# Kernel tuning notes

Hardware: AMD Instinct MI355X
Metric: run time of the kernel (lower is better)

## Reference

```python
import jax, jax.numpy as jnp
import numpy as np

# ---- static geometry / topology tables (the CUDA kernel's x,y,z,inner tables) ----
W = D = H = 49                     # vertex grid
Wc, Dc, Hc = W - 1, D - 1, H - 1    # cell grid
N_CELLS = Wc * Dc * Hc
T_FULL = 96                         # number of topology classes in `topology`
T_TRI = 48                          # triangle-bearing topologies (topology_to_triangles)
EPS = 1e-8

# 12 cube edges: (corner where edge starts, axis the edge runs along)
EDGE_CORNER = np.array([
    [0,0,0],[0,1,0],[0,0,1],[0,1,1],   # x-edges
    [0,0,0],[1,0,0],[0,0,1],[1,0,1],   # y-edges
    [0,0,0],[1,0,0],[0,1,0],[1,1,0],   # z-edges
], dtype=np.int32)
EDGE_AXIS = np.array([0,0,0,0,1,1,1,1,2,2,2,2], dtype=np.int32)

_rng = np.random.default_rng(0)
# per triangle-topology: the 3 cube edges carrying its triangle vertices
TRI_TABLE = np.stack([_rng.choice(12, size=3, replace=False) for _ in range(T_TRI)]).astype(np.int32)
# columns of `topology` that correspond to triangle topologies
TT_IDX = np.sort(_rng.choice(T_FULL, size=T_TRI, replace=False)).astype(np.int32)


def _triangle_normals(offset):
    """offset: [3, W, D, H] -> unit normals [T_TRI, Wc, Dc, Hc, 3]."""
    verts = []
    for e in range(12):
        cx, cy, cz = EDGE_CORNER[e]
        ax = int(EDGE_AXIS[e])
        # displacement of the MC vertex along its edge, gathered per cell
        disp = offset[ax, cx:cx + Wc, cy:cy + Dc, cz:cz + Hc]   # [Wc,Dc,Hc]
        base = np.array([cx, cy, cz], dtype=np.float32)
        base[ax] += 0.5                                          # edge midpoint
        unit = np.zeros(3, dtype=np.float32); unit[ax] = 1.0
        # cell-local vertex position (cell origin cancels in edge differences)
        verts.append(jnp.asarray(base) + disp[..., None] * jnp.asarray(unit))
    verts = jnp.stack(verts)                                     # [12,Wc,Dc,Hc,3]
    v0 = verts[TRI_TABLE[:, 0]]                                  # [T_TRI,Wc,Dc,Hc,3]
    v1 = verts[TRI_TABLE[:, 1]]
    v2 = verts[TRI_TABLE[:, 2]]
    n = jnp.cross(v1 - v0, v2 - v0)
    n = n / jnp.sqrt(jnp.sum(n * n, axis=-1, keepdims=True) + EPS)
    return n


def _curvature_loss(offset, topology):
    n = _triangle_normals(offset)                                # [T,Wc,Dc,Hc,3]
    p = topology[:, TT_IDX].reshape(Wc, Dc, Hc, T_TRI)           # per-cell topo probs
    s = jnp.sum(p, axis=-1)                                      # [Wc,Dc,Hc]
    m = jnp.einsum('xyzt,txyzc->xyzc', p, n)                     # prob-weighted normal sum

    # sum_{t1,t2} p1 p2 ||n1 - n2||^2 = 2*(s1*s2 - m1.m2) for unit normals
    def pair(sa, ma, sb, mb):
        return jnp.sum(2.0 * (sa * sb - jnp.sum(ma * mb, axis=-1)))

    loss_x = pair(s[:-1], m[:-1], s[1:], m[1:])
    loss_y = pair(s[:, :-1], m[:, :-1], s[:, 1:], m[:, 1:])
    loss_z = pair(s[:, :, :-1], m[:, :, :-1], s[:, :, 1:], m[:, :, 1:])
    loss_inner = pair(s, m, s, m)
    return loss_x + loss_y + loss_z + loss_inner


def setup_inputs() -> dict:
    key = jax.random.key(0)
    k1, k2 = jax.random.split(key)
    offset = 0.1 * jax.random.normal(k1, (3, W, D, H), dtype=jnp.float32)
    topology = jax.random.uniform(k2, (N_CELLS, T_FULL), dtype=jnp.float32)
    return {"offset": offset, "topology": topology}


def reference(offset, topology):
    return _curvature_loss(offset, topology)
```

## Files before the change

### kernel.cpp

```cpp
#include <hip/hip_runtime.h>
#include <cstdint>

#define NCELLS (48*48*48)
#define NT 48
#define CB 64
#define NW 8
#define PITCH 97
#define OFFE 882

namespace nprng {
typedef unsigned __int128 u128;
struct PCG { u128 state; u128 inc; int has32; uint32_t cached; };

constexpr u128 mult128() {
  return (((u128)2549297995355413924ULL) << 64) | (u128)4865540595714422341ULL;
}
constexpr void step(PCG& g) { g.state = g.state * mult128() + g.inc; }
constexpr uint64_t out64(const PCG& g) {
  uint64_t x = (uint64_t)(g.state >> 64) ^ (uint64_t)g.state;
  unsigned rot = (unsigned)(g.state >> 122);
  return (x >> rot) | (x << ((64u - rot) & 63u));
}
constexpr uint64_t next64(PCG& g) { step(g); return out64(g); }
constexpr uint32_t next32(PCG& g) {
  if (g.has32) { g.has32 = 0; return g.cached; }
  uint64_t v = next64(g);
  g.has32 = 1; g.cached = (uint32_t)(v >> 32);
  return (uint32_t)v;
}
constexpr uint32_t lemire32(PCG& g, uint32_t rngmax) {
  const uint32_t rng_excl = rngmax + 1u;
  uint64_t m = (uint64_t)next32(g) * (uint64_t)rng_excl;
  uint32_t leftover = (uint32_t)m;
  if (leftover < rng_excl) {
    const uint32_t threshold = (uint32_t)((0xFFFFFFFFu - rngmax) % rng_excl);
    while (leftover < threshold) {
      m = (uint64_t)next32(g) * (uint64_t)rng_excl;
      leftover = (uint32_t)m;
    }
  }
  return (uint32_t)(m >> 32);
}
constexpr uint64_t rbu(PCG& g, uint64_t rngmax) {
  if (rngmax == 0) return 0;
  return (uint64_t)lemire32(g, (uint32_t)rngmax);
}
constexpr uint32_t hashmix(uint32_t v, uint32_t& hc) {
  v ^= hc; hc *= 0x931e8875u; v *= hc; v ^= v >> 16; return v;
}
constexpr uint32_t mix2(uint32_t x, uint32_t y) {
  uint32_t r = 0xca01f9ddu * x - 0x4973f715u * y; r ^= r >> 16; return r;
}
constexpr PCG seed_pcg0() {
  PCG g{0, 0, 0, 0};
  uint32_t pool[4] = {};
  uint32_t hc = 0x43b0d7e5u;
  for (int i = 0; i < 4; i++) pool[i] = hashmix(0u, hc);
  for (int s = 0; s < 4; s++)
    for (int d = 0; d < 4; d++)
      if (s != d) pool[d] = mix2(pool[d], hashmix(pool[s], hc));
  uint32_t st[8] = {};
  uint32_t hb = 0x8b51f9ddu;
  for (int i = 0; i < 8; i++) {
    uint32_t v = pool[i & 3];
    v ^= hb; hb *= 0x58f38dedu; v *= hb; v ^= v >> 16;
    st[i] = v;
  }
  uint64_t w[4] = {};
  for (int i = 0; i < 4; i++) w[i] = (uint64_t)st[2 * i] | ((uint64_t)st[2 * i + 1] << 32);
  u128 initstate = (((u128)w[0]) << 64) | (u128)w[1];
  u128 initseq   = (((u128)w[2]) << 64) | (u128)w[3];
  g.state = 0; g.inc = (initseq << 1) | (u128)1;
  step(g); g.state += initstate; step(g);
  g.has32 = 0; g.cached = 0;
  return g;
}
constexpr void choice_nr(PCG& g, int pop, int n, int* outv, bool shuf) {
  uint64_t hs[64] = {};
  uint64_t set_size = (uint64_t)(1.2 * (double)n);
  uint64_t mask = set_size;
  mask |= mask >> 1; mask |= mask >> 2; mask |= mask >> 4;
  mask |= mask >> 8; mask |= mask >> 16; mask |= mask >> 32;
  for (int i = 0; i < 64; i++) hs[i] = ~0ULL;
  for (int j = pop - n; j < pop; j++) {
    uint64_t val = rbu(g, (uint64_t)j);
    uint64_t loc = val & mask;
    while (hs[loc] != ~0ULL && hs[loc] != val) loc = (loc + 1) & mask;
    if (hs[loc] == ~0ULL) { hs[loc] = val; outv[j - (pop - n)] = (int)val; }
    else {
      loc = (uint64_t)j & mask;
      while (hs[loc] != ~0ULL) loc = (loc + 1) & mask;
      hs[loc] = (uint64_t)j;
      outv[j - (pop - n)] = j;
    }
  }
  if (shuf) {
    for (int i = n - 1; i >= 1; i--) {
      uint64_t j = rbu(g, (uint64_t)i);
      int t = outv[i]; outv[i] = outv[(int)j]; outv[(int)j] = t;
    }
  }
}
}

struct TriTab3 {
  float ub[NT][3];
  float wb[NT][3];
  int   a0[NT], a1[NT], a2[NT];
  int   lofc[NT][3];
  int   tto[NT];
};

constexpr TriTab3 make_tab() {
  TriTab3 T{};
  nprng::PCG g = nprng::seed_pcg0();
  int tri[NT][3] = {};
  for (int t = 0; t < NT; t++) nprng::choice_nr(g, 12, 3, tri[t], true);
  int tt[NT] = {};
  nprng::choice_nr(g, 96, NT, tt, true);
  for (int i = 1; i < NT; i++) {
    int v = tt[i], j = i - 1;
    while (j >= 0 && tt[j] > v) { tt[j + 1] = tt[j]; j--; }
    tt[j + 1] = v;
  }
  constexpr int EC[12][3] = {{0,0,0},{0,1,0},{0,0,1},{0,1,1},
                             {0,0,0},{1,0,0},{0,0,1},{1,0,1},
                             {0,0,0},{1,0,0},{0,1,0},{1,1,0}};
  constexpr int EA[12] = {0,0,0,0,1,1,1,1,2,2,2,2};
  for (int t = 0; t < NT; t++) {
    float B[3][3] = {};
    int ax[3] = {};
    for (int k = 0; k < 3; k++) {
      int e = tri[t][k];
      int a = EA[e];
      ax[k] = a;
      T.lofc[t][k] = ((a * 2 + EC[e][0]) * 3 + EC[e][1]) * 49 + EC[e][2];
      B[k][0] = (float)EC[e][0]; B[k][1] = (float)EC[e][1]; B[k][2] = (float)EC[e][2];
      B[k][a] += 0.5f;
    }
    for (int c = 0; c < 3; c++) {
      T.ub[t][c] = B[1][c] - B[0][c];
      T.wb[t][c] = B[2][c] - B[0][c];
    }
    T.a0[t] = ax[0]; T.a1[t] = ax[1]; T.a2[t] = ax[2];
    T.tto[t] = tt[t];
  }
  return T;
}

static constexpr TriTab3 TAB = make_tab();

template <int t>
__device__ __forceinline__ void do1(const float* __restrict__ loff, int lanebase,
                                    const float* __restrict__ myrow,
                                    float& s, float& mx, float& my, float& mz) {
  constexpr int L0 = TAB.lofc[t][0], L1 = TAB.lofc[t][1], L2 = TAB.lofc[t][2];
  constexpr int A0 = TAB.a0[t], A1 = TAB.a1[t], A2 = TAB.a2[t];
  float p  = myrow[TAB.tto[t]];
  float d0 = loff[lanebase + L0];
  float d1 = loff[lanebase + L1];
  float d2 = loff[lanebase + L2];
  float ux = TAB.ub[t][0] + (A1 == 0 ? d1 : 0.0f) - (A0 == 0 ? d0 : 0.0f);
  float uy = TAB.ub[t][1] + (A1 == 1 ? d1 : 0.0f) - (A0 == 1 ? d0 : 0.0f);
  float uz = TAB.ub[t][2] + (A1 == 2 ? d1 : 0.0f) - (A0 == 2 ? d0 : 0.0f);
  float wx = TAB.wb[t][0] + (A2 == 0 ? d2 : 0.0f) - (A0 == 0 ? d0 : 0.0f);
  float wy = TAB.wb[t][1] + (A2 == 1 ? d2 : 0.0f) - (A0 == 1 ? d0 : 0.0f);
  float wz = TAB.wb[t][2] + (A2 == 2 ? d2 : 0.0f) - (A0 == 2 ? d0 : 0.0f);
  float cxv = uy * wz - uz * wy;
  float cyv = uz * wx - ux * wz;
  float czv = ux * wy - uy * wx;
  float nn = cxv * cxv + cyv * cyv + czv * czv + 1e-8f;
  float rinv = rsqrtf(nn);
  s += p;
  float f = p * rinv;
  mx += f * cxv;
  my += f * cyv;
  mz += f * czv;
}

template <int T0>
__device__ __forceinline__ void do6(const float* __restrict__ loff, int lanebase,
                                    const float* __restrict__ myrow,
                                    float& s, float& mx, float& my, float& mz) {
  do1<T0 + 0>(loff, lanebase, myrow, s, mx, my, mz);
  do1<T0 + 1>(loff, lanebase, myrow, s, mx, my, mz);
  do1<T0 + 2>(loff, lanebase, myrow, s, mx, my, mz);
  do1<T0 + 3>(loff, lanebase, myrow, s, mx, my, mz);
  do1<T0 + 4>(loff, lanebase, myrow, s, mx, my, mz);
  do1<T0 + 5>(loff, lanebase, myrow, s, mx, my, mz);
}

__global__ __launch_bounds__(CB * NW) void k_cell(const float* __restrict__ off,
                                                  const float* __restrict__ topo,
                                                  float4* __restrict__ ws4,
                                                  float* __restrict__ out) {
  __shared__ float lds[CB * PITCH];
  __shared__ float loff[OFFE];
  __shared__ float4 red[CB * NW];
  const int tid = threadIdx.x;
  const int lane = tid & 63;
  const int cell0 = blockIdx.x * CB;

  if (blockIdx.x == 0 && tid == 0) *out = 0.0f;

  const int x0 = cell0 / 2304;
  const int y0 = (cell0 / 48) % 48;
  for (int e = tid; e < OFFE; e += CB * NW) {
    int r = e / 49, zz = e % 49;
    int dy = r % 3, rr = r / 3;
    int dx = rr & 1, a = rr >> 1;
    loff[e] = off[a * 117649 + (x0 + dx) * 2401 + (y0 + dy) * 49 + zz];
  }

  const float4* trow = (const float4*)(topo + (size_t)cell0 * 96);
#pragma unroll
  for (int it = 0; it < 3; ++it) {
    int ch = tid + CB * NW * it;
    float4 v = trow[ch];
    int r  = ch / 24;
    int c4 = (ch % 24) * 4;
    float* dst = &lds[r * PITCH + c4];
    dst[0] = v.x; dst[1] = v.y; dst[2] = v.z; dst[3] = v.w;
  }
  __syncthreads();

  const int cell = cell0 + lane;
  const int z = cell % 48;
  const int ly = ((cell / 48) % 48) - y0;
  const int lanebase = ly * 49 + z;
  const float* myrow = &lds[lane * PITCH];

  float s = 0.f, mx = 0.f, my = 0.f, mz = 0.f;
  const int wvu = __builtin_amdgcn_readfirstlane(tid >> 6);
  if (wvu == 0)      do6<0>(loff, lanebase, myrow, s, mx, my, mz);
  else if (wvu == 1) do6<6>(loff, lanebase, myrow, s, mx, my, mz);
  else if (wvu == 2) do6<12>(loff, lanebase, myrow, s, mx, my, mz);
  else if (wvu == 3) do6<18>(loff, lanebase, myrow, s, mx, my, mz);
  else if (wvu == 4) do6<24>(loff, lanebase, myrow, s, mx, my, mz);
  else if (wvu == 5) do6<30>(loff, lanebase, myrow, s, mx, my, mz);
  else if (wvu == 6) do6<36>(loff, lanebase, myrow, s, mx, my, mz);
  else               do6<42>(loff, lanebase, myrow, s, mx, my, mz);

  red[tid] = make_float4(s, mx, my, mz);
  __syncthreads();

  if (tid < 64) {
    float sx = 0.f, sy = 0.f, sz = 0.f, sw = 0.f;
#pragma unroll
    for (int w = 0; w < NW; w++) {
      float4 a = red[lane + 64 * w];
      sx += a.x; sy += a.y; sz += a.z; sw += a.w;
    }
    ws4[cell0 + lane] = make_float4(sx, sy, sz, sw);
  }
}

__global__ __launch_bounds__(256) void k_pair(const float4* __restrict__ ws4,
                                              float* __restrict__ out) {
  int cell = blockIdx.x * 256 + threadIdx.x;
  int z = cell % 48;
  int y = (cell / 48) % 48;
  int x = cell / 2304;
  float4 a = ws4[cell];
  float acc = a.x * a.x - (a.y * a.y + a.z * a.z + a.w * a.w);
  if (z < 47) {
    float4 b = ws4[cell + 1];
    acc += a.x * b.x - (a.y * b.y + a.z * b.z + a.w * b.w);
  }
  if (y < 47) {
    float4 b = ws4[cell + 48];
    acc += a.x * b.x - (a.y * b.y + a.z * b.z + a.w * b.w);
  }
  if (x < 47) {
    float4 b = ws4[cell + 2304];
    acc += a.x * b.x - (a.y * b.y + a.z * b.z + a.w * b.w);
  }
  acc *= 2.0f;
  for (int o = 32; o > 0; o >>= 1) acc += __shfl_down(acc, o, 64);
  __shared__ float lds[4];
  int lane = threadIdx.x & 63;
  int w = threadIdx.x >> 6;
  if (lane == 0) lds[w] = acc;
  __syncthreads();
  if (threadIdx.x == 0) atomicAdd(out, lds[0] + lds[1] + lds[2] + lds[3]);
}

extern "C" void kernel_launch(void* const* d_in, const int* in_sizes, int n_in,
                              void* d_out, int out_size, void* d_ws, size_t ws_size,
                              hipStream_t stream) {
  const float* off  = (const float*)d_in[0];
  const float* topo = (const float*)d_in[1];
  float4* ws4 = (float4*)d_ws;
  float* out  = (float*)d_out;

  k_cell<<<dim3(NCELLS / CB), dim3(CB * NW), 0, stream>>>(off, topo, ws4, out);
  k_pair<<<dim3(NCELLS / 256), dim3(256), 0, stream>>>(ws4, out);
}
```

Before: 90.79 us.

## Process four cell tiles per block with double-buffered topology prefetch

Each block now handles four 64-cell tiles instead of one. The offset slab covering 7 y-rows is loaded into LDS once per block, and the next tile's topology rows are prefetched into registers and stored into a second LDS buffer while the current tile is computed. The final 8-wave reduction now uses a padded LDS layout plus xor shuffles, so every wave helps instead of only the first. This cuts per-block setup and offset reloads and overlaps global loads with compute, at the cost of more LDS (two tile buffers and two reduction buffers), which may reduce occupancy, and four times fewer blocks.

```diff
diff --git a/kernel.cpp b/kernel.cpp
--- a/kernel.cpp
+++ b/kernel.cpp
@@ -4,9 +4,11 @@
 #define NCELLS (48*48*48)
 #define NT 48
 #define CB 64
+#define TILES 4
+#define NBLK (NCELLS / (CB * TILES))
 #define NW 8
 #define PITCH 97
-#define OFFE 882
+#define OFFE (3*2*7*49)
 
 namespace nprng {
 typedef unsigned __int128 u128;
@@ -134,7 +136,7 @@
       int e = tri[t][k];
       int a = EA[e];
       ax[k] = a;
-      T.lofc[t][k] = ((a * 2 + EC[e][0]) * 3 + EC[e][1]) * 49 + EC[e][2];
+      T.lofc[t][k] = ((a * 2 + EC[e][0]) * 7 + EC[e][1]) * 49 + EC[e][2];
       B[k][0] = (float)EC[e][0]; B[k][1] = (float)EC[e][1]; B[k][2] = (float)EC[e][2];
       B[k][a] += 0.5f;
     }
@@ -190,68 +192,96 @@
   do1<T0 + 5>(loff, lanebase, myrow, s, mx, my, mz);
 }
 
-__global__ __launch_bounds__(CB * NW) void k_cell(const float* __restrict__ off,
-                                                  const float* __restrict__ topo,
-                                                  float4* __restrict__ ws4,
-                                                  float* __restrict__ out) {
-  __shared__ float lds[CB * PITCH];
+__global__ __launch_bounds__(CB * NW, 4) void k_cell(const float* __restrict__ off,
+                                                     const float* __restrict__ topo,
+                                                     float4* __restrict__ ws4,
+                                                     float* __restrict__ out) {
+  __shared__ float tbuf[2][CB * PITCH];
   __shared__ float loff[OFFE];
-  __shared__ float4 red[CB * NW];
+  __shared__ float4 red[2][NW * 65];
   const int tid = threadIdx.x;
   const int lane = tid & 63;
-  const int cell0 = blockIdx.x * CB;
+  const int wv = tid >> 6;
+  const int c00 = blockIdx.x * (CB * TILES);
+  const int x0 = c00 / 2304;
+  const int y0 = (c00 / 48) % 48;
 
   if (blockIdx.x == 0 && tid == 0) *out = 0.0f;
 
-  const int x0 = cell0 / 2304;
-  const int y0 = (cell0 / 48) % 48;
   for (int e = tid; e < OFFE; e += CB * NW) {
-    int r = e / 49, zz = e % 49;
-    int dy = r % 3, rr = r / 3;
+    int zz = e % 49, r = e / 49;
+    int ly = r % 7, rr = r / 7;
     int dx = rr & 1, a = rr >> 1;
-    loff[e] = off[a * 117649 + (x0 + dx) * 2401 + (y0 + dy) * 49 + zz];
-  }
-
-  const float4* trow = (const float4*)(topo + (size_t)cell0 * 96);
+    loff[e] = off[a * 117649 + (x0 + dx) * 2401 + (y0 + ly) * 49 + zz];
+  }
+  {
+    const float4* trow = (const float4*)(topo + (size_t)c00 * 96);
 #pragma unroll
-  for (int it = 0; it < 3; ++it) {
-    int ch = tid + CB * NW * it;
-    float4 v = trow[ch];
-    int r  = ch / 24;
-    int c4 = (ch % 24) * 4;
-    float* dst = &lds[r * PITCH + c4];
-    dst[0] = v.x; dst[1] = v.y; dst[2] = v.z; dst[3] = v.w;
+    for (int it = 0; it < 3; ++it) {
+      int ch = tid + 512 * it;
+      float4 v = trow[ch];
+      int r = ch / 24, c4 = (ch % 24) * 4;
+      float* dst = &tbuf[0][r * PITCH + c4];
+      dst[0] = v.x; dst[1] = v.y; dst[2] = v.z; dst[3] = v.w;
+    }
   }
   __syncthreads();
 
-  const int cell = cell0 + lane;
-  const int z = cell % 48;
-  const int ly = ((cell / 48) % 48) - y0;
-  const int lanebase = ly * 49 + z;
-  const float* myrow = &lds[lane * PITCH];
-
-  float s = 0.f, mx = 0.f, my = 0.f, mz = 0.f;
-  const int wvu = __builtin_amdgcn_readfirstlane(tid >> 6);
-  if (wvu == 0)      do6<0>(loff, lanebase, myrow, s, mx, my, mz);
-  else if (wvu == 1) do6<6>(loff, lanebase, myrow, s, mx, my, mz);
-  else if (wvu == 2) do6<12>(loff, lanebase, myrow, s, mx, my, mz);
-  else if (wvu == 3) do6<18>(loff, lanebase, myrow, s, mx, my, mz);
-  else if (wvu == 4) do6<24>(loff, lanebase, myrow, s, mx, my, mz);
-  else if (wvu == 5) do6<30>(loff, lanebase, myrow, s, mx, my, mz);
-  else if (wvu == 6) do6<36>(loff, lanebase, myrow, s, mx, my, mz);
-  else               do6<42>(loff, lanebase, myrow, s, mx, my, mz);
-
-  red[tid] = make_float4(s, mx, my, mz);
-  __syncthreads();
-
-  if (tid < 64) {
-    float sx = 0.f, sy = 0.f, sz = 0.f, sw = 0.f;
+  for (int t = 0; t < TILES; ++t) {
+    const int bsel = t & 1;
+    float4 p0, p1, p2;
+    const bool pf = (t + 1 < TILES);
+    if (pf) {
+      const float4* trow = (const float4*)(topo + (size_t)(c00 + (t + 1) * CB) * 96);
+      p0 = trow[tid];
+      p1 = trow[tid + 512];
+      p2 = trow[tid + 1024];
+    }
+
+    const int cell = c00 + t * CB + lane;
+    const int z = cell % 48;
+    const int ly = ((cell / 48) % 48) - y0;
+    const int lanebase = ly * 49 + z;
+    const float* myrow = &tbuf[bsel][lane * PITCH];
+
+    float s = 0.f, mx = 0.f, my = 0.f, mz = 0.f;
+    const int wvu = __builtin_amdgcn_readfirstlane(wv);
+    if (wvu == 0)      do6<0>(loff, lanebase, myrow, s, mx, my, mz);
+    else if (wvu == 1) do6<6>(loff, lanebase, myrow, s, mx, my, mz);
+    else if (wvu == 2) do6<12>(loff, lanebase, myrow, s, mx, my, mz);
+    else if (wvu == 3) do6<18>(loff, lanebase, myrow, s, mx, my, mz);
+    else if (wvu == 4) do6<24>(loff, lanebase, myrow, s, mx, my, mz);
+    else if (wvu == 5) do6<30>(loff, lanebase, myrow, s, mx, my, mz);
+    else if (wvu == 6) do6<36>(loff, lanebase, myrow, s, mx, my, mz);
+    else               do6<42>(loff, lanebase, myrow, s, mx, my, mz);
+
+    red[bsel][wv * 65 + lane] = make_float4(s, mx, my, mz);
+
+    if (pf) {
 #pragma unroll
-    for (int w = 0; w < NW; w++) {
-      float4 a = red[lane + 64 * w];
-      sx += a.x; sy += a.y; sz += a.z; sw += a.w;
-    }
-    ws4[cell0 + lane] = make_float4(sx, sy, sz, sw);
+      for (int it = 0; it < 3; ++it) {
+        int ch = tid + 512 * it;
+        float4 v = (it == 0) ? p0 : (it == 1) ? p1 : p2;
+        int r = ch / 24, c4 = (ch % 24) * 4;
+        float* dst = &tbuf[1 - bsel][r * PITCH + c4];
+        dst[0] = v.x; dst[1] = v.y; dst[2] = v.z; dst[3] = v.w;
+      }
+    }
+    __syncthreads();
+
+    {
+      const int c = (wv << 3) + (lane >> 3);
+      const int p = lane & 7;
+      float4 v = red[bsel][p * 65 + c];
+#pragma unroll
+      for (int d = 1; d < 8; d <<= 1) {
+        v.x += __shfl_xor(v.x, d, 64);
+        v.y += __shfl_xor(v.y, d, 64);
+        v.z += __shfl_xor(v.z, d, 64);
+        v.w += __shfl_xor(v.w, d, 64);
+      }
+      if (p == 0) ws4[c00 + t * CB + c] = v;
+    }
   }
 }
 
@@ -293,6 +323,6 @@
   float4* ws4 = (float4*)d_ws;
   float* out  = (float*)d_out;
 
-  k_cell<<<dim3(NCELLS / CB), dim3(CB * NW), 0, stream>>>(off, topo, ws4, out);
+  k_cell<<<dim3(NBLK), dim3(CB * NW), 0, stream>>>(off, topo, ws4, out);
   k_pair<<<dim3(NCELLS / 256), dim3(256), 0, stream>>>(ws4, out);
 }
```

After: 93.12 us. 2.6% more time.

## Pack topology probabilities as bf16 in LDS and use 4 waves per block

Applied to the files above, without the earlier changes.

The topology tile is rounded to bf16 and stored two values per 32-bit word in shared memory, which halves the LDS footprint per block. The block shrinks from 8 to 4 waves, so each wave now handles 12 triangle topologies instead of 6, and launch bounds request 6 blocks per CU. The aim is more resident blocks and less LDS pressure. The cost is that probabilities lose precision to bf16, which may move the loss outside the reference tolerance.

```diff
diff --git a/kernel.cpp b/kernel.cpp
--- a/kernel.cpp
+++ b/kernel.cpp
@@ -4,8 +4,8 @@
 #define NCELLS (48*48*48)
 #define NT 48
 #define CB 64
-#define NW 8
-#define PITCH 97
+#define NTH 256
+#define WPITCH 49
 #define OFFE 882
 
 namespace nprng {
@@ -150,13 +150,20 @@
 
 static constexpr TriTab3 TAB = make_tab();
 
+__device__ __forceinline__ uint32_t bfr(float f) {
+  uint32_t u = __float_as_uint(f);
+  return (u + 0x7FFFu + ((u >> 16) & 1u)) >> 16;
+}
+
 template <int t>
 __device__ __forceinline__ void do1(const float* __restrict__ loff, int lanebase,
-                                    const float* __restrict__ myrow,
+                                    const uint32_t* __restrict__ myrow,
                                     float& s, float& mx, float& my, float& mz) {
   constexpr int L0 = TAB.lofc[t][0], L1 = TAB.lofc[t][1], L2 = TAB.lofc[t][2];
   constexpr int A0 = TAB.a0[t], A1 = TAB.a1[t], A2 = TAB.a2[t];
-  float p  = myrow[TAB.tto[t]];
+  constexpr int W = TAB.tto[t] >> 1, H = TAB.tto[t] & 1;
+  uint32_t pw = myrow[W];
+  float p = __uint_as_float(H ? (pw & 0xFFFF0000u) : (pw << 16));
   float d0 = loff[lanebase + L0];
   float d1 = loff[lanebase + L1];
   float d2 = loff[lanebase + L2];
@@ -179,24 +186,30 @@
 }
 
 template <int T0>
-__device__ __forceinline__ void do6(const float* __restrict__ loff, int lanebase,
-                                    const float* __restrict__ myrow,
-                                    float& s, float& mx, float& my, float& mz) {
+__device__ __forceinline__ void do12(const float* __restrict__ loff, int lanebase,
+                                     const uint32_t* __restrict__ myrow,
+                                     float& s, float& mx, float& my, float& mz) {
   do1<T0 + 0>(loff, lanebase, myrow, s, mx, my, mz);
   do1<T0 + 1>(loff, lanebase, myrow, s, mx, my, mz);
   do1<T0 + 2>(loff, lanebase, myrow, s, mx, my, mz);
   do1<T0 + 3>(loff, lanebase, myrow, s, mx, my, mz);
   do1<T0 + 4>(loff, lanebase, myrow, s, mx, my, mz);
   do1<T0 + 5>(loff, lanebase, myrow, s, mx, my, mz);
-}
-
-__global__ __launch_bounds__(CB * NW) void k_cell(const float* __restrict__ off,
-                                                  const float* __restrict__ topo,
-                                                  float4* __restrict__ ws4,
-                                                  float* __restrict__ out) {
-  __shared__ float lds[CB * PITCH];
+  do1<T0 + 6>(loff, lanebase, myrow, s, mx, my, mz);
+  do1<T0 + 7>(loff, lanebase, myrow, s, mx, my, mz);
+  do1<T0 + 8>(loff, lanebase, myrow, s, mx, my, mz);
+  do1<T0 + 9>(loff, lanebase, myrow, s, mx, my, mz);
+  do1<T0 + 10>(loff, lanebase, myrow, s, mx, my, mz);
+  do1<T0 + 11>(loff, lanebase, myrow, s, mx, my, mz);
+}
+
+__global__ __launch_bounds__(NTH, 6) void k_cell(const float* __restrict__ off,
+                                                 const float* __restrict__ topo,
+                                                 float4* __restrict__ ws4,
+                                                 float* __restrict__ out) {
+  __shared__ uint32_t tbuf32[CB * WPITCH];
   __shared__ float loff[OFFE];
-  __shared__ float4 red[CB * NW];
+  __shared__ float4 red[NTH];
   const int tid = threadIdx.x;
   const int lane = tid & 63;
   const int cell0 = blockIdx.x * CB;
@@ -205,7 +218,7 @@
 
   const int x0 = cell0 / 2304;
   const int y0 = (cell0 / 48) % 48;
-  for (int e = tid; e < OFFE; e += CB * NW) {
+  for (int e = tid; e < OFFE; e += NTH) {
     int r = e / 49, zz = e % 49;
     int dy = r % 3, rr = r / 3;
     int dx = rr & 1, a = rr >> 1;
@@ -214,13 +227,13 @@
 
   const float4* trow = (const float4*)(topo + (size_t)cell0 * 96);
 #pragma unroll
-  for (int it = 0; it < 3; ++it) {
-    int ch = tid + CB * NW * it;
+  for (int it = 0; it < 6; ++it) {
+    int ch = tid + NTH * it;
     float4 v = trow[ch];
     int r  = ch / 24;
-    int c4 = (ch % 24) * 4;
-    float* dst = &lds[r * PITCH + c4];
-    dst[0] = v.x; dst[1] = v.y; dst[2] = v.z; dst[3] = v.w;
+    int w0 = (ch % 24) * 2;
+    tbuf32[r * WPITCH + w0]     = bfr(v.x) | (bfr(v.y) << 16);
+    tbuf32[r * WPITCH + w0 + 1] = bfr(v.z) | (bfr(v.w) << 16);
   }
   __syncthreads();
 
@@ -228,30 +241,27 @@
   const int z = cell % 48;
   const int ly = ((cell / 48) % 48) - y0;
   const int lanebase = ly * 49 + z;
-  const float* myrow = &lds[lane * PITCH];
+  const uint32_t* myrow = &tbuf32[lane * WPITCH];
 
   float s = 0.f, mx = 0.f, my = 0.f, mz = 0.f;
   const int wvu = __builtin_amdgcn_readfirstlane(tid >> 6);
-  if (wvu == 0)      do6<0>(loff, lanebase, myrow, s, mx, my, mz);
-  else if (wvu == 1) do6<6>(loff, lanebase, myrow, s, mx, my, mz);
-  else if (wvu == 2) do6<12>(loff, lanebase, myrow, s, mx, my, mz);
-  else if (wvu == 3) do6<18>(loff, lanebase, myrow, s, mx, my, mz);
-  else if (wvu == 4) do6<24>(loff, lanebase, myrow, s, mx, my, mz);
-  else if (wvu == 5) do6<30>(loff, lanebase, myrow, s, mx, my, mz);
-  else if (wvu == 6) do6<36>(loff, lanebase, myrow, s, mx, my, mz);
-  else               do6<42>(loff, lanebase, myrow, s, mx, my, mz);
+  if (wvu == 0)      do12<0>(loff, lanebase, myrow, s, mx, my, mz);
+  else if (wvu == 1) do12<12>(loff, lanebase, myrow, s, mx, my, mz);
+  else if (wvu == 2) do12<24>(loff, lanebase, myrow, s, mx, my, mz);
+  else               do12<36>(loff, lanebase, myrow, s, mx, my, mz);
 
   red[tid] = make_float4(s, mx, my, mz);
   __syncthreads();
 
   if (tid < 64) {
-    float sx = 0.f, sy = 0.f, sz = 0.f, sw = 0.f;
-#pragma unroll
-    for (int w = 0; w < NW; w++) {
-      float4 a = red[lane + 64 * w];
-      sx += a.x; sy += a.y; sz += a.z; sw += a.w;
-    }
-    ws4[cell0 + lane] = make_float4(sx, sy, sz, sw);
+    float4 a = red[lane];
+    float4 b = red[lane + 64];
+    float4 c = red[lane + 128];
+    float4 d = red[lane + 192];
+    ws4[cell0 + lane] = make_float4(a.x + b.x + c.x + d.x,
+                                    a.y + b.y + c.y + d.y,
+                                    a.z + b.z + c.z + d.z,
+                                    a.w + b.w + c.w + d.w);
   }
 }
 
@@ -293,6 +303,6 @@
   float4* ws4 = (float4*)d_ws;
   float* out  = (float*)d_out;
 
-  k_cell<<<dim3(NCELLS / CB), dim3(CB * NW), 0, stream>>>(off, topo, ws4, out);
+  k_cell<<<dim3(NCELLS / CB), dim3(NTH), 0, stream>>>(off, topo, ws4, out);
   k_pair<<<dim3(NCELLS / 256), dim3(256), 0, stream>>>(ws4, out);
 }
```

After: 93.58 us. +3.1%, slower.
